# Optimization experiments

Measured on AMD Instinct MI355X. Metric: run time of the kernel, lower is better.

## Reference

```python
import jax, jax.numpy as jnp
import numpy as np
from jax import lax

DWT_SCALE = 0.5
IDWT_SCALE = 1.0
PAD = 2  # (kernel_size-1)//2 for k=5


def haar_dwt(x, s):
    """x: [B,C,H,W] -> (ll, lh, hl, hh) each [B,C,H/2,W/2]. 2x2 Haar, scale s."""
    a = x[..., 0::2, 0::2]
    b = x[..., 0::2, 1::2]
    c = x[..., 1::2, 0::2]
    d = x[..., 1::2, 1::2]
    ll = s * (a + b + c + d)
    lh = s * (a + b - c - d)
    hl = s * (a - b + c - d)
    hh = s * (a - b - c + d)
    return ll, lh, hl, hh


def haar_idwt(ll, lh, hl, hh, s):
    """Inverse of haar_dwt when s_dwt * s_idwt_total = 0.5. Returns [B,C,2H,2W]."""
    a = s * (ll + lh + hl + hh)
    b = s * (ll + lh - hl - hh)
    c = s * (ll - lh + hl - hh)
    d = s * (ll - lh - hl + hh)
    B, C, H2, W2 = ll.shape
    top = jnp.stack([a, b], axis=-1).reshape(B, C, H2, 2 * W2)  # even rows
    bot = jnp.stack([c, d], axis=-1).reshape(B, C, H2, 2 * W2)  # odd rows
    return jnp.stack([top, bot], axis=-2).reshape(B, C, 2 * H2, 2 * W2)


def conv2d(x, w, pad):
    return lax.conv_general_dilated(
        x, w, window_strides=(1, 1), padding=[(pad, pad), (pad, pad)],
        dimension_numbers=("NCHW", "OIHW", "NCHW"))


def setup_inputs() -> dict:
    key = jax.random.key(0)
    kx, k0, k1, k2, kb = jax.random.split(key, 5)
    C, K = 64, 5
    x = jax.random.normal(kx, (8, C, 256, 256), dtype=jnp.float32)
    # kaiming_uniform-ish small init to keep 3-level recursion numerically tame
    scale = 0.02
    w0 = jax.random.normal(k0, (4 * C, 4 * C, K, K), dtype=jnp.float32) * scale
    w1 = jax.random.normal(k1, (4 * C, 4 * C, K, K), dtype=jnp.float32) * scale
    w2 = jax.random.normal(k2, (4 * C, 4 * C, K, K), dtype=jnp.float32) * scale
    bias = jax.random.normal(kb, (C,), dtype=jnp.float32) * 0.01
    return {"x": x, "w0": w0, "w1": w1, "w2": w2, "bias": bias}


def reference(x, w0, w1, w2, bias):
    weights = [w0, w1, w2]
    idwt_s = DWT_SCALE * IDWT_SCALE  # perfect reconstruction pair
    curr = x
    ll_levels, high_levels = [], []
    for w in weights:
        ll, lh, hl, hh = haar_dwt(curr, DWT_SCALE)
        curr = ll  # pre-conv LL feeds the next level
        B, C, H2, W2 = ll.shape
        stacked = jnp.stack([ll, lh, hl, hh], axis=2).reshape(B, 4 * C, H2, W2)
        y = conv2d(stacked, w, PAD)  # [B, 4*Co, H2, W2]
        y = y.reshape(B, -1, 4, H2, W2)
        ll_levels.append(y[:, :, 0])
        high_levels.append(y[:, :, 1:])
    next_ll = jnp.zeros_like(ll_levels[-1])
    for ll_t, h_t in zip(reversed(ll_levels), reversed(high_levels)):
        ll = ll_t + next_ll
        next_ll = haar_idwt(ll, h_t[:, :, 0], h_t[:, :, 1], h_t[:, :, 2], idwt_s)
    return next_ll + bias.reshape(1, -1, 1, 1)
```

## Files before the change

kernel.cpp:

```cpp
#include <hip/hip_runtime.h>


typedef unsigned short u16;
typedef __attribute__((ext_vector_type(8))) __bf16 bf16x8;
typedef __attribute__((ext_vector_type(4))) float f32x4;

__device__ __forceinline__ u16 f2bf(float f) {
  union { float f; unsigned u; } v; v.f = f;
  unsigned r = v.u + 0x7fffu + ((v.u >> 16) & 1u);
  return (u16)(r >> 16);
}
__device__ __forceinline__ float bf2f(u16 u) {
  union { unsigned u; float f; } v; v.u = ((unsigned)u) << 16;
  return v.f;
}

typedef const unsigned int __attribute__((address_space(1)))* gas1_t;
typedef unsigned int __attribute__((address_space(3)))* gas3_t;
__device__ __forceinline__ void gload16(const void* g, void* l) {
  __builtin_amdgcn_global_load_lds((gas1_t)g, (gas3_t)l, 16, 0, 0);
}

__global__ void k_wtrans3(const float* __restrict__ wa, const float* __restrict__ wb_,
                          const float* __restrict__ wc, u16* __restrict__ oa,
                          u16* __restrict__ ob, u16* __restrict__ oc) {
  const float* w = (blockIdx.y == 0) ? wa : (blockIdx.y == 1) ? wb_ : wc;
  u16* o = (blockIdx.y == 0) ? oa : (blockIdx.y == 1) ? ob : oc;
  int co = blockIdx.x;
  int ci = threadIdx.x;
  const float* src = w + ((long)co * 256 + ci) * 25;
  float v[25];
#pragma unroll
  for (int tp = 0; tp < 25; ++tp) v[tp] = src[tp];
#pragma unroll
  for (int tp = 0; tp < 25; ++tp)
    o[((long)tp * 256 + co) * 256 + ci] = f2bf(v[tp]);
}

__global__ void k_border(u16* __restrict__ st, int B_, int H2, int W2) {
  int PW = W2 + 4;
  int npix = 4 * PW + 4 * H2;
  int gid = blockIdx.x * blockDim.x + threadIdx.x;
  int pid = gid >> 6, lane = gid & 63;
  if (pid >= B_ * npix) return;
  int b = pid / npix, p = pid % npix;
  int row, col;
  if (p < 2 * PW) { row = p / PW; col = p % PW; }
  else if (p < 4 * PW) { int q = p - 2 * PW; row = H2 + 2 + q / PW; col = q % PW; }
  else { int q = p - 4 * PW; row = 2 + (q >> 2); int c4 = q & 3; col = (c4 < 2) ? c4 : W2 + c4; }
  long base = (((long)b * (H2 + 4) + row) * PW + col) * 256 + lane * 4;
  *(ushort4*)(st + base) = make_ushort4(0, 0, 0, 0);
}

__global__ void k_dwt(const float* __restrict__ in, u16* __restrict__ st,
                      float* __restrict__ ll, int B_, int H2, int W2) {
  int idx = blockIdx.x * blockDim.x + threadIdx.x;
  int W2h = W2 >> 1;
  int total = B_ * 64 * H2 * W2h;
  if (idx >= total) return;
  int w2h = idx % W2h; int t2 = idx / W2h;
  int h2 = t2 % H2; t2 /= H2;
  int c = t2 % 64; int b = t2 / 64;
  int w2 = w2h * 2;
  const float* r0 = in + (((long)(b * 64 + c) * (2 * H2) + 2 * h2) * (2 * W2)) + 2 * w2;
  const float* r1 = r0 + 2 * W2;
  float4 tp = *(const float4*)r0;
  float4 bt = *(const float4*)r1;
  float ll0 = 0.5f * (tp.x + tp.y + bt.x + bt.y);
  float lh0 = 0.5f * (tp.x + tp.y - bt.x - bt.y);
  float hl0 = 0.5f * (tp.x - tp.y + bt.x - bt.y);
  float hh0 = 0.5f * (tp.x - tp.y - bt.x + bt.y);
  float ll1 = 0.5f * (tp.z + tp.w + bt.z + bt.w);
  float lh1 = 0.5f * (tp.z + tp.w - bt.z - bt.w);
  float hl1 = 0.5f * (tp.z - tp.w + bt.z - bt.w);
  float hh1 = 0.5f * (tp.z - tp.w - bt.z + bt.w);
  long sbase = (((long)b * (H2 + 4) + (h2 + 2)) * (W2 + 4) + (w2 + 2)) * 256 + 4 * c;
  *(ushort4*)(st + sbase)       = make_ushort4(f2bf(ll0), f2bf(lh0), f2bf(hl0), f2bf(hh0));
  *(ushort4*)(st + sbase + 256) = make_ushort4(f2bf(ll1), f2bf(lh1), f2bf(hl1), f2bf(hh1));
  long lbase = (((long)(b * 64 + c) * H2) + h2) * W2 + w2;
  *(float2*)(ll + lbase) = make_float2(ll0, ll1);
}

__global__ __launch_bounds__(1024, 4) void k_conv32(
    const u16* __restrict__ st, const u16* __restrict__ wt, u16* __restrict__ out,
    int H2, int W2, int ktot, int nsplit) {
  __shared__ __align__(16) char smem[65536];
  const int t = threadIdx.x;
  const int lane = t & 63;
  const int wv = t >> 6;
  const int wm = wv >> 2, wn = wv & 3;
  const int nwg = gridDim.x;
  const int bid = blockIdx.x;
  const int lb = (bid & 7) * (nwg >> 3) + (bid >> 3);
  const int m0 = lb * 256;
  const int PW = W2 + 4;
  const int spl = blockIdx.y;
  const int kk0 = (spl * ktot) / nsplit;
  const int kk1 = ((spl + 1) * ktot) / nsplit;
  u16* yo = out + (long)spl * ((long)nwg * 256) * 256;

  const char* baseA;
  {
    int m = m0 + (t >> 2);
    int w = m % W2; int q = m / W2;
    int hh = q % H2; int b = q / H2;
    long sp = ((long)(b * (H2 + 4) + hh + 2) * PW + (w + 2));
    baseA = (const char*)(st + sp * 256 + (t & 3) * 8);
  }
  const char* baseB = (const char*)(wt + (t >> 2) * 256 + (t & 3) * 8);

  f32x4 acc[4][4];
#pragma unroll
  for (int i = 0; i < 4; ++i)
#pragma unroll
    for (int j = 0; j < 4; ++j) acc[i][j] = f32x4{0.f, 0.f, 0.f, 0.f};

  int va = (wm * 64 + (lane & 15)) * 64 + ((lane >> 4) << 4);
  int vb = 16384 + (wn * 64 + (lane & 15)) * 64 + ((lane >> 4) << 4);

  bf16x8 a01[2], a23[2], bb[4];

  auto offsets = [&](int kk, long& oA, long& oB) {
    int tap = kk >> 3, cic = kk & 7;
    int dy = tap / 5 - 2, dx = tap % 5 - 2;
    oA = ((long)(dy * PW + dx) * 256 + cic * 32) * 2;
    oB = ((long)tap * 65536 + cic * 32) * 2;
  };
  auto stage2 = [&](long oA, long oB, int dsto) {
    gload16(baseA + oA, smem + dsto + wv * 1024);
    gload16(baseB + oB, smem + dsto + 16384 + wv * 1024);
  };

#define LDEND { a01[0] = *(const bf16x8*)(smem + va);                 \
    a01[1] = *(const bf16x8*)(smem + va + 1024);                      \
    _Pragma("unroll") for (int j = 0; j < 4; ++j)                     \
      bb[j] = *(const bf16x8*)(smem + vb + j * 1024); }
#define MM2(A2, I0)                                                   \
  _Pragma("unroll") for (int i2 = 0; i2 < 2; ++i2)                    \
  _Pragma("unroll") for (int j = 0; j < 4; ++j)                       \
    acc[(I0) + i2][j] = __builtin_amdgcn_mfma_f32_16x16x32_bf16(      \
        A2[i2], bb[j], acc[(I0) + i2][j], 0, 0, 0);

  long oA, oB;
  offsets(kk0, oA, oB);
  stage2(oA, oB, 0);
  offsets(kk0 + 1, oA, oB);
  stage2(oA, oB, 32768);
  asm volatile("s_waitcnt vmcnt(2)" ::: "memory");
  __builtin_amdgcn_s_barrier();
  LDEND

  int curo = 0;
  for (int kt = kk0; kt < kk1; ++kt) {
    const bool stg = (kt + 2) < kk1;
    const bool rd1 = (kt + 1) < kk1;
    a23[0] = *(const bf16x8*)(smem + va + 2048);
    a23[1] = *(const bf16x8*)(smem + va + 3072);
    va ^= 32768; vb ^= 32768;
    __builtin_amdgcn_s_barrier();
    asm volatile("s_waitcnt lgkmcnt(2)" ::: "memory");
    __builtin_amdgcn_sched_barrier(0);
    __builtin_amdgcn_s_setprio(1);
    MM2(a01, 0)
    __builtin_amdgcn_s_setprio(0);
    if (rd1) { asm volatile("s_waitcnt vmcnt(0)" ::: "memory"); }
    __builtin_amdgcn_s_barrier();
    asm volatile("s_waitcnt lgkmcnt(0)" ::: "memory");
    __builtin_amdgcn_sched_barrier(0);
    __builtin_amdgcn_s_setprio(1);
    MM2(a23, 2)
    __builtin_amdgcn_s_setprio(0);
    __builtin_amdgcn_sched_barrier(0);
    if (stg) { offsets(kt + 2, oA, oB); stage2(oA, oB, curo); }
    if (rd1) { LDEND }
    __builtin_amdgcn_sched_barrier(0);
    curo ^= 32768;
  }
#undef MM2
#undef LDEND

#pragma unroll
  for (int i = 0; i < 4; ++i) {
    int mloc = m0 + wm * 64 + i * 16 + (lane >> 4) * 4;
#pragma unroll
    for (int j = 0; j < 4; ++j) {
      int nloc = wn * 64 + j * 16 + (lane & 15);
#pragma unroll
      for (int r = 0; r < 4; ++r)
        yo[(long)(mloc + r) * 256 + nloc] = f2bf(acc[i][j][r]);
    }
  }
}

__global__ void k_idwt(const u16* __restrict__ P, long psz, int ns,
                       const float* __restrict__ nll, const float* __restrict__ bias,
                       float* __restrict__ out, int B_, int H2, int W2) {
  int idx = blockIdx.x * blockDim.x + threadIdx.x;
  int W2h = W2 >> 1;
  int total = B_ * 64 * H2 * W2h;
  if (idx >= total) return;
  int w2h = idx % W2h; int t2 = idx / W2h;
  int h2 = t2 % H2; t2 /= H2;
  int c = t2 % 64; int b = t2 / 64;
  int w2 = w2h * 2;
  long ybase = (((long)b * H2 + h2) * W2 + w2) * 256 + 4 * c;
  float s[8] = {0.f, 0.f, 0.f, 0.f, 0.f, 0.f, 0.f, 0.f};
  for (int k = 0; k < ns; ++k) {
    const u16* p = P + (long)k * psz + ybase;
    ushort4 q0 = *(const ushort4*)(p);
    ushort4 q1 = *(const ushort4*)(p + 256);
    s[0] += bf2f(q0.x); s[1] += bf2f(q0.y); s[2] += bf2f(q0.z); s[3] += bf2f(q0.w);
    s[4] += bf2f(q1.x); s[5] += bf2f(q1.y); s[6] += bf2f(q1.z); s[7] += bf2f(q1.w);
  }
  float llv0 = s[0], lh0 = s[1], hl0 = s[2], hh0 = s[3];
  float llv1 = s[4], lh1 = s[5], hl1 = s[6], hh1 = s[7];
  if (nll) {
    float2 nv = *(const float2*)(nll + (((long)(b * 64 + c) * H2 + h2) * W2 + w2));
    llv0 += nv.x; llv1 += nv.y;
  }
  float bv = bias ? bias[c] : 0.f;
  float a0 = 0.5f * (llv0 + lh0 + hl0 + hh0) + bv;
  float b0 = 0.5f * (llv0 + lh0 - hl0 - hh0) + bv;
  float c0 = 0.5f * (llv0 - lh0 + hl0 - hh0) + bv;
  float d0 = 0.5f * (llv0 - lh0 - hl0 + hh0) + bv;
  float a1 = 0.5f * (llv1 + lh1 + hl1 + hh1) + bv;
  float b1 = 0.5f * (llv1 + lh1 - hl1 - hh1) + bv;
  float c1 = 0.5f * (llv1 - lh1 + hl1 - hh1) + bv;
  float d1 = 0.5f * (llv1 - lh1 - hl1 + hh1) + bv;
  long obase = (((long)(b * 64 + c) * (2 * H2) + 2 * h2) * (2 * W2)) + 2 * w2;
  *(float4*)(out + obase)          = make_float4(a0, b0, a1, b1);
  *(float4*)(out + obase + 2 * W2) = make_float4(c0, d0, c1, d1);
}

constexpr size_t WBF_SZ1 = 25ull * 256 * 256 * 2;
constexpr size_t OFF_WBF = 0;
constexpr size_t OFF_S0  = 3 * WBF_SZ1;
constexpr size_t S0_SZ   = 8ull * 132 * 132 * 256 * 2;
constexpr size_t OFF_L0  = OFF_S0 + S0_SZ;
constexpr size_t OFF_Y0  = OFF_L0 + 8ull * 64 * 128 * 128 * 4;
constexpr size_t REL_S1 = 0;
constexpr size_t REL_L1 = 8ull * 68 * 68 * 256 * 2;
constexpr size_t REL_S2 = REL_L1 + 8ull * 64 * 64 * 64 * 4;
constexpr size_t REL_P2 = REL_S2 + 8ull * 36 * 36 * 256 * 2;
constexpr size_t REL_N2 = 0;
constexpr size_t REL_N1 = 8ull * 64 * 64 * 64 * 4;
constexpr size_t REL_L2 = 0;

extern "C" void kernel_launch(void* const* d_in, const int* in_sizes, int n_in,
                              void* d_out, int out_size, void* d_ws, size_t ws_size,
                              hipStream_t stream) {
  const float* x    = (const float*)d_in[0];
  const float* w0   = (const float*)d_in[1];
  const float* w1   = (const float*)d_in[2];
  const float* w2   = (const float*)d_in[3];
  const float* bias = (const float*)d_in[4];
  float* out = (float*)d_out;
  char* ws = (char*)d_ws;

  u16* wbf0 = (u16*)(ws + OFF_WBF);
  u16* wbf1 = (u16*)(ws + OFF_WBF + WBF_SZ1);
  u16* wbf2 = (u16*)(ws + OFF_WBF + 2 * WBF_SZ1);
  u16* s0   = (u16*)(ws + OFF_S0);
  u16* s1   = (u16*)(ws + OFF_S0 + REL_S1);
  float* l1 = (float*)(ws + OFF_S0 + REL_L1);
  u16* s2   = (u16*)(ws + OFF_S0 + REL_S2);
  u16* P2   = (u16*)(ws + OFF_S0 + REL_P2);
  float* n2 = (float*)(ws + OFF_S0 + REL_N2);
  float* n1 = (float*)(ws + OFF_S0 + REL_N1);
  float* l2 = (float*)(ws + OFF_S0 + REL_L2);
  float* l0 = (float*)(ws + OFF_L0);
  u16* P1   = (u16*)(ws + OFF_L0);
  u16* y0   = (u16*)(ws + OFF_Y0);

  k_wtrans3<<<dim3(256, 3), 256, 0, stream>>>(w0, w1, w2, wbf0, wbf1, wbf2);

  k_border<<<2080, 256, 0, stream>>>(s0, 8, 128, 128);
  k_dwt<<<16384, 256, 0, stream>>>(x, s0, l0, 8, 128, 128);
  k_conv32<<<dim3(512, 1), 1024, 0, stream>>>(s0, wbf0, y0, 128, 128, 200, 1);

  k_border<<<1056, 256, 0, stream>>>(s1, 8, 64, 64);
  k_border<<<544, 256, 0, stream>>>(s2, 8, 32, 32);

  k_dwt<<<4096, 256, 0, stream>>>(l0, s1, l1, 8, 64, 64);
  k_conv32<<<dim3(128, 2), 1024, 0, stream>>>(s1, wbf1, P1, 64, 64, 200, 2);

  k_dwt<<<1024, 256, 0, stream>>>(l1, s2, l2, 8, 32, 32);
  k_conv32<<<dim3(32, 8), 1024, 0, stream>>>(s2, wbf2, P2, 32, 32, 200, 8);

  k_idwt<<<1024, 256, 0, stream>>>(P2, 2097152L, 8, nullptr, nullptr, n2, 8, 32, 32);
  k_idwt<<<4096, 256, 0, stream>>>(P1, 8388608L, 2, n2, nullptr, n1, 8, 64, 64);
  k_idwt<<<16384, 256, 0, stream>>>(y0, 33554432L, 1, n1, bias, out, 8, 128, 128);
}
```

Baseline: 713.5 us.

## Restructure conv GEMM: 512 threads, per-wave register-held weights, swizzled LDS A tiles

The implicit-GEMM conv kernel now runs 512 threads per block, with each wave computing a 128x64 output tile (8x4 MFMA accumulators). The K step doubles to 64 channels, which halves the k-iterations from 200 to 100. Weights (B) are loaded straight from global memory into registers, double-buffered across k-tiles. Only the activation (A) tile is staged through LDS, using an XOR swizzle to avoid bank conflicts. The aim is less LDS traffic and fewer barriers per MFMA, at the cost of much higher register pressure (launch bounds 512,1) and uncached global reads of the weights.

Result: slower. 923.3 us (+29.4%).

```diff
diff --git a/kernel.cpp b/kernel.cpp
--- a/kernel.cpp
+++ b/kernel.cpp
@@ -81,7 +81,7 @@
   *(float2*)(ll + lbase) = make_float2(ll0, ll1);
 }
 
-__global__ __launch_bounds__(1024, 4) void k_conv32(
+__global__ __launch_bounds__(512, 1) void k_convB(
     const u16* __restrict__ st, const u16* __restrict__ wt, u16* __restrict__ out,
     int H2, int W2, int ktot, int nsplit) {
   __shared__ __align__(16) char smem[65536];
@@ -99,89 +99,112 @@
   const int kk1 = ((spl + 1) * ktot) / nsplit;
   u16* yo = out + (long)spl * ((long)nwg * 256) * 256;
 
-  const char* baseA;
-  {
-    int m = m0 + (t >> 2);
+  const int trow = t >> 3;
+  const int srcci = ((t & 7) ^ (trow & 7)) * 8;
+  const char* baseA[4];
+#pragma unroll
+  for (int u = 0; u < 4; ++u) {
+    int m = m0 + u * 64 + trow;
     int w = m % W2; int q = m / W2;
     int hh = q % H2; int b = q / H2;
     long sp = ((long)(b * (H2 + 4) + hh + 2) * PW + (w + 2));
-    baseA = (const char*)(st + sp * 256 + (t & 3) * 8);
-  }
-  const char* baseB = (const char*)(wt + (t >> 2) * 256 + (t & 3) * 8);
-
-  f32x4 acc[4][4];
-#pragma unroll
-  for (int i = 0; i < 4; ++i)
+    baseA[u] = (const char*)(st + sp * 256 + srcci);
+  }
+  const char* baseB = (const char*)(wt + ((long)(wn * 64 + (lane & 15))) * 256 + (lane >> 4) * 8);
+
+  f32x4 acc[8][4];
+#pragma unroll
+  for (int i = 0; i < 8; ++i)
 #pragma unroll
     for (int j = 0; j < 4; ++j) acc[i][j] = f32x4{0.f, 0.f, 0.f, 0.f};
 
-  int va = (wm * 64 + (lane & 15)) * 64 + ((lane >> 4) << 4);
-  int vb = 16384 + (wn * 64 + (lane & 15)) * 64 + ((lane >> 4) << 4);
-
-  bf16x8 a01[2], a23[2], bb[4];
-
-  auto offsets = [&](int kk, long& oA, long& oB) {
-    int tap = kk >> 3, cic = kk & 7;
+  const int kq = (lane >> 4) * 16;
+  const int sw = (lane & 7) << 4;
+  const int kx0 = kq ^ sw;
+  const int kx1 = (64 + kq) ^ sw;
+  const int aBase = (wm * 128 + (lane & 15)) * 128;
+
+  bf16x8 a[4][2], bbA[4][2], bbB[4][2];
+
+  auto offA = [&](int kk) -> long {
+    int tap = kk >> 2, cic = kk & 3;
     int dy = tap / 5 - 2, dx = tap % 5 - 2;
-    oA = ((long)(dy * PW + dx) * 256 + cic * 32) * 2;
-    oB = ((long)tap * 65536 + cic * 32) * 2;
+    return ((long)(dy * PW + dx) * 256 + cic * 64) * 2;
   };
-  auto stage2 = [&](long oA, long oB, int dsto) {
-    gload16(baseA + oA, smem + dsto + wv * 1024);
-    gload16(baseB + oB, smem + dsto + 16384 + wv * 1024);
+  auto stageA4 = [&](long off, int dsto) {
+    char* d = smem + dsto + wv * 1024;
+#pragma unroll
+    for (int u = 0; u < 4; ++u) gload16(baseA[u] + off, d + u * 8192);
   };
 
-#define LDEND { a01[0] = *(const bf16x8*)(smem + va);                 \
-    a01[1] = *(const bf16x8*)(smem + va + 1024);                      \
-    _Pragma("unroll") for (int j = 0; j < 4; ++j)                     \
-      bb[j] = *(const bf16x8*)(smem + vb + j * 1024); }
-#define MM2(A2, I0)                                                   \
-  _Pragma("unroll") for (int i2 = 0; i2 < 2; ++i2)                    \
-  _Pragma("unroll") for (int j = 0; j < 4; ++j)                       \
-    acc[(I0) + i2][j] = __builtin_amdgcn_mfma_f32_16x16x32_bf16(      \
-        A2[i2], bb[j], acc[(I0) + i2][j], 0, 0, 0);
-
-  long oA, oB;
-  offsets(kk0, oA, oB);
-  stage2(oA, oB, 0);
-  offsets(kk0 + 1, oA, oB);
-  stage2(oA, oB, 32768);
-  asm volatile("s_waitcnt vmcnt(2)" ::: "memory");
+#define LOADB(kk, BB) { int tap_ = (kk) >> 2, cic_ = (kk) & 3;                  \
+    long ob_ = ((long)tap_ * 65536 + cic_ * 64) * 2;                            \
+    _Pragma("unroll") for (int j = 0; j < 4; ++j)                               \
+    _Pragma("unroll") for (int ks = 0; ks < 2; ++ks)                            \
+      BB[j][ks] = *(const bf16x8*)(baseB + j * 8192 + ob_ + ks * 64); }
+#define LDA(H, P) { _Pragma("unroll") for (int i = 0; i < 4; ++i) {             \
+    a[i][0] = *(const bf16x8*)((P) + aBase + (H) * 8192 + i * 2048 + kx0);      \
+    a[i][1] = *(const bf16x8*)((P) + aBase + (H) * 8192 + i * 2048 + kx1); } }
+#define MMH(BB, I0)                                                             \
+  _Pragma("unroll") for (int i = 0; i < 4; ++i)                                 \
+  _Pragma("unroll") for (int j = 0; j < 4; ++j)                                 \
+  _Pragma("unroll") for (int ks = 0; ks < 2; ++ks)                              \
+    acc[(I0) + i][j] = __builtin_amdgcn_mfma_f32_16x16x32_bf16(                 \
+        a[i][ks], BB[j][ks], acc[(I0) + i][j], 0, 0, 0);
+
+#define KTILE(BBC, BBN, kt)                                                     \
+  { const bool st2 = (kt) + 2 < kk1; const bool ld1 = (kt) + 1 < kk1;           \
+    char* cur = smem + curo; char* alt = smem + (curo ^ 32768);                 \
+    asm volatile("s_waitcnt lgkmcnt(0)" ::: "memory");                          \
+    __builtin_amdgcn_sched_barrier(0);                                          \
+    __builtin_amdgcn_s_setprio(1);                                              \
+    MMH(BBC, 0)                                                                 \
+    __builtin_amdgcn_s_setprio(0);                                              \
+    __builtin_amdgcn_sched_barrier(0);                                          \
+    LDA(1, cur)                                                                 \
+    asm volatile("s_waitcnt lgkmcnt(0)" ::: "memory");                          \
+    __builtin_amdgcn_sched_barrier(0);                                          \
+    __builtin_amdgcn_s_setprio(1);                                              \
+    MMH(BBC, 4)                                                                 \
+    __builtin_amdgcn_s_setprio(0);                                              \
+    __builtin_amdgcn_sched_barrier(0);                                          \
+    if (ld1) { LOADB((kt) + 1, BBN) }                                           \
+    if (ld1) { asm volatile("s_waitcnt vmcnt(8)" ::: "memory"); }               \
+    else     { asm volatile("s_waitcnt vmcnt(0)" ::: "memory"); }               \
+    __builtin_amdgcn_s_barrier();                                               \
+    if (st2) { stageA4(offA((kt) + 2), curo); }                                 \
+    if (ld1) { LDA(0, alt) }                                                    \
+    if (ld1) {                                                                  \
+      if (st2) { asm volatile("s_waitcnt vmcnt(4)" ::: "memory"); }             \
+      else     { asm volatile("s_waitcnt vmcnt(0)" ::: "memory"); }             \
+    }                                                                           \
+    __builtin_amdgcn_sched_barrier(0);                                          \
+    curo ^= 32768; }
+
+  stageA4(offA(kk0), 0);
+  stageA4(offA(kk0 + 1), 32768);
+  LOADB(kk0, bbA)
+  asm volatile("s_waitcnt vmcnt(0)" ::: "memory");
   __builtin_amdgcn_s_barrier();
-  LDEND
-
   int curo = 0;
-  for (int kt = kk0; kt < kk1; ++kt) {
-    const bool stg = (kt + 2) < kk1;
-    const bool rd1 = (kt + 1) < kk1;
-    a23[0] = *(const bf16x8*)(smem + va + 2048);
-    a23[1] = *(const bf16x8*)(smem + va + 3072);
-    va ^= 32768; vb ^= 32768;
-    __builtin_amdgcn_s_barrier();
-    asm volatile("s_waitcnt lgkmcnt(2)" ::: "memory");
-    __builtin_amdgcn_sched_barrier(0);
-    __builtin_amdgcn_s_setprio(1);
-    MM2(a01, 0)
-    __builtin_amdgcn_s_setprio(0);
-    if (rd1) { asm volatile("s_waitcnt vmcnt(0)" ::: "memory"); }
-    __builtin_amdgcn_s_barrier();
-    asm volatile("s_waitcnt lgkmcnt(0)" ::: "memory");
-    __builtin_amdgcn_sched_barrier(0);
-    __builtin_amdgcn_s_setprio(1);
-    MM2(a23, 2)
-    __builtin_amdgcn_s_setprio(0);
-    __builtin_amdgcn_sched_barrier(0);
-    if (stg) { offsets(kt + 2, oA, oB); stage2(oA, oB, curo); }
-    if (rd1) { LDEND }
-    __builtin_amdgcn_sched_barrier(0);
-    curo ^= 32768;
-  }
-#undef MM2
-#undef LDEND
-
-#pragma unroll
-  for (int i = 0; i < 4; ++i) {
-    int mloc = m0 + wm * 64 + i * 16 + (lane >> 4) * 4;
+  LDA(0, smem)
+
+  int kt = kk0;
+  while (kt < kk1) {
+    KTILE(bbA, bbB, kt)
+    ++kt;
+    if (kt >= kk1) break;
+    KTILE(bbB, bbA, kt)
+    ++kt;
+  }
+#undef KTILE
+#undef MMH
+#undef LDA
+#undef LOADB
+
+#pragma unroll
+  for (int i = 0; i < 8; ++i) {
+    int mloc = m0 + wm * 128 + i * 16 + (lane >> 4) * 4;
 #pragma unroll
     for (int j = 0; j < 4; ++j) {
       int nloc = wn * 64 + j * 16 + (lane & 15);
@@ -276,16 +299,16 @@
 
   k_border<<<2080, 256, 0, stream>>>(s0, 8, 128, 128);
   k_dwt<<<16384, 256, 0, stream>>>(x, s0, l0, 8, 128, 128);
-  k_conv32<<<dim3(512, 1), 1024, 0, stream>>>(s0, wbf0, y0, 128, 128, 200, 1);
+  k_convB<<<dim3(512, 1), 512, 0, stream>>>(s0, wbf0, y0, 128, 128, 100, 1);
 
   k_border<<<1056, 256, 0, stream>>>(s1, 8, 64, 64);
   k_border<<<544, 256, 0, stream>>>(s2, 8, 32, 32);
 
   k_dwt<<<4096, 256, 0, stream>>>(l0, s1, l1, 8, 64, 64);
-  k_conv32<<<dim3(128, 2), 1024, 0, stream>>>(s1, wbf1, P1, 64, 64, 200, 2);
+  k_convB<<<dim3(128, 2), 512, 0, stream>>>(s1, wbf1, P1, 64, 64, 100, 2);
 
   k_dwt<<<1024, 256, 0, stream>>>(l1, s2, l2, 8, 32, 32);
-  k_conv32<<<dim3(32, 8), 1024, 0, stream>>>(s2, wbf2, P2, 32, 32, 200, 8);
+  k_convB<<<dim3(32, 8), 512, 0, stream>>>(s2, wbf2, P2, 32, 32, 100, 8);
 
   k_idwt<<<1024, 256, 0, stream>>>(P2, 2097152L, 8, nullptr, nullptr, n2, 8, 32, 32);
   k_idwt<<<4096, 256, 0, stream>>>(P1, 8388608L, 2, n2, nullptr, n1, 8, 64, 64);
```
